# Optimization experiments

Measured on AMD Instinct MI355X. Metric: run time of the kernel, lower is better.

## Reference

```python
import jax, jax.numpy as jnp
import numpy as np

NUM_HEADS = 12
HEAD_DIM = 64
LOGIT_SCALE_MAX = 4.605170185988092  # log(1/0.01), open_clip default
EPS = 1e-12  # F.normalize eps


def setup_inputs() -> dict:
    key = jax.random.key(0)
    ks = jax.random.split(key, 8)
    N, L, C = 2, 2048, 768
    return {
        "x": jax.random.normal(ks[0], (N, L, C), dtype=jnp.float32),
        "in_proj_w": jax.random.normal(ks[1], (3 * C, C), dtype=jnp.float32) * 0.02,
        "in_proj_b": jax.random.normal(ks[2], (3 * C,), dtype=jnp.float32) * 0.02,
        "logit_scale": jax.random.normal(ks[3], (NUM_HEADS, 1, 1), dtype=jnp.float32),
        "learned_scale": jnp.ones((NUM_HEADS,), dtype=jnp.float32),
        "out_proj_w": jax.random.normal(ks[4], (C, C), dtype=jnp.float32) * 0.02,
        "out_proj_b": jax.random.normal(ks[5], (C,), dtype=jnp.float32) * 0.02,
        "attn_mask": jnp.zeros((L, L), dtype=jnp.float32),
    }


def _l2norm(t):
    # F.normalize(dim=-1): x / max(||x||, eps)
    n = jnp.linalg.norm(t, axis=-1, keepdims=True)
    return t / jnp.maximum(n, EPS)


def reference(x, in_proj_w, in_proj_b, logit_scale, learned_scale,
              out_proj_w, out_proj_b, attn_mask):
    N, L, C = x.shape
    H, D = NUM_HEADS, HEAD_DIM
    # packed QKV projection: [N, L, 3C]
    qkv = jnp.einsum("nlc,fc->nlf", x, in_proj_w) + in_proj_b
    q, k, v = jnp.split(qkv, 3, axis=-1)
    # [N, L, C] -> [N, H, L, D]
    to_heads = lambda t: t.reshape(N, L, H, D).transpose(0, 2, 1, 3)
    q, k, v = to_heads(q), to_heads(k), to_heads(v)
    # cosine attention with clamped exp logit scale per head
    attn = jnp.einsum("nhld,nhmd->nhlm", _l2norm(q), _l2norm(k))
    ls = jnp.exp(jnp.minimum(logit_scale, LOGIT_SCALE_MAX))  # [H,1,1]
    attn = attn * ls[None]  # broadcast over [N,H,L,L]
    attn = attn + attn_mask  # additive mask [L,L]
    attn = jax.nn.softmax(attn, axis=-1)
    out = jnp.einsum("nhlm,nhmd->nhld", attn, v)
    # learned per-head output scale
    out = out * learned_scale[None, :, None, None]
    # [N,H,L,D] -> [N,L,C]
    out = out.transpose(0, 2, 1, 3).reshape(N, L, C)
    out = jnp.einsum("nlc,fc->nlf", out, out_proj_w) + out_proj_b
    return out
```

## Files before the change

### kernel.cpp

```cpp
#include <hip/hip_runtime.h>
#include <math.h>

#define NB   2
#define SEQ  2048
#define CH   768
#define NH   12
#define HD   64
#define F3   2304
#define LSMAX 4.605170185988092f

typedef _Float16 f16;
typedef __attribute__((ext_vector_type(8))) _Float16 f16x8;
typedef __attribute__((ext_vector_type(4))) _Float16 f16x4;
typedef __attribute__((ext_vector_type(4))) float f32x4;

#define QSZ   3145728
#define OATT  (3 * QSZ)
#define XHOFF 12582912
#define W1OFF 15728640
#define W2OFF 17498112
#define MOFF  18087936

#define PIT  72
#define PPIT 76
#define GP   40

__global__ __launch_bounds__(256) void cvt_f16(const float* __restrict__ X,
                                               const float* __restrict__ W1,
                                               const float* __restrict__ W2,
                                               const float* __restrict__ M,
                                               f16* __restrict__ Xh,
                                               f16* __restrict__ W1h,
                                               f16* __restrict__ W2h,
                                               f16* __restrict__ Mh)
{
    int tid = blockIdx.x * 256 + threadIdx.x;
    const float* src; f16* dst; int n4;
    switch (blockIdx.y) {
        case 0:  src = X;  dst = Xh;  n4 = 786432;  break;
        case 1:  src = W1; dst = W1h; n4 = 442368;  break;
        case 2:  src = W2; dst = W2h; n4 = 147456;  break;
        default: src = M;  dst = Mh;  n4 = 1048576; break;
    }
    if (tid < n4) {
        float4 v = ((const float4*)src)[tid];
        f16x4 o = {(f16)v.x, (f16)v.y, (f16)v.z, (f16)v.w};
        ((f16x4*)dst)[tid] = o;
    }
}

__global__ __launch_bounds__(256, 3) void qkv_gemm(const f16* __restrict__ Xh,
                                                   const f16* __restrict__ Wh,
                                                   const float* __restrict__ bias,
                                                   const float* __restrict__ logit_scale,
                                                   f16* __restrict__ qkv16)
{
    __shared__ f16 As[128 * GP];
    __shared__ f16 Bs[128 * GP];
    const int t    = threadIdx.x;
    const int w    = t >> 6;
    const int lane = t & 63;
    const int quad = lane >> 4;
    const int sub  = lane & 15;
    const int wm   = w & 1, wn = w >> 1;
    const int f0   = blockIdx.x * 128;
    const int m0   = blockIdx.y * 128;
    const int srow = t >> 1;
    const int sk   = (t & 1) * 16;

    const f16* ag = Xh + (size_t)(m0 + srow) * CH + sk;
    const f16* bg = Wh + (size_t)(f0 + srow) * CH + sk;
    f16x8 a0 = *(const f16x8*)(ag);
    f16x8 a1 = *(const f16x8*)(ag + 8);
    f16x8 b0 = *(const f16x8*)(bg);
    f16x8 b1 = *(const f16x8*)(bg + 8);

    f32x4 acc[4][4];
#pragma unroll
    for (int i = 0; i < 4; ++i)
#pragma unroll
        for (int j = 0; j < 4; ++j) acc[i][j] = (f32x4){0.f, 0.f, 0.f, 0.f};

    for (int k0 = 0; k0 < CH; k0 += 32) {
        __syncthreads();
        *(f16x8*)&As[srow * GP + sk + 0] = a0;
        *(f16x8*)&As[srow * GP + sk + 8] = a1;
        *(f16x8*)&Bs[srow * GP + sk + 0] = b0;
        *(f16x8*)&Bs[srow * GP + sk + 8] = b1;
        __syncthreads();
        if (k0 + 32 < CH) {
            a0 = *(const f16x8*)(ag + k0 + 32);
            a1 = *(const f16x8*)(ag + k0 + 40);
            b0 = *(const f16x8*)(bg + k0 + 32);
            b1 = *(const f16x8*)(bg + k0 + 40);
        }
        f16x8 af[4], bf[4];
#pragma unroll
        for (int i = 0; i < 4; ++i) {
            af[i] = *(const f16x8*)&As[(wm * 64 + i * 16 + sub) * GP + quad * 8];
            bf[i] = *(const f16x8*)&Bs[(wn * 64 + i * 16 + sub) * GP + quad * 8];
        }
#pragma unroll
        for (int i = 0; i < 4; ++i)
#pragma unroll
            for (int j = 0; j < 4; ++j)
                acc[i][j] = __builtin_amdgcn_mfma_f32_16x16x32_f16(af[i], bf[j], acc[i][j], 0, 0, 0);
    }

    const int t3 = f0 / CH;
    const int h  = ((f0 + wn * 64) % CH) >> 6;
    f16* dst = qkv16 + (size_t)t3 * QSZ;
    float lsv = (t3 == 0) ? __expf(fminf(logit_scale[h], LSMAX)) : 1.0f;
    float bb[4];
#pragma unroll
    for (int j = 0; j < 4; ++j) bb[j] = bias[f0 + wn * 64 + j * 16 + sub];
#pragma unroll
    for (int i = 0; i < 4; ++i) {
#pragma unroll
        for (int r = 0; r < 4; ++r) {
            int m = m0 + wm * 64 + i * 16 + quad * 4 + r;
            int n = m >> 11, l = m & 2047;
            float v[4];
#pragma unroll
            for (int j = 0; j < 4; ++j) v[j] = acc[i][j][r] + bb[j];
            float scale = 1.0f;
            if (t3 < 2) {
                float ss = v[0] * v[0] + v[1] * v[1] + v[2] * v[2] + v[3] * v[3];
#pragma unroll
                for (int mk = 1; mk < 16; mk <<= 1) ss += __shfl_xor(ss, mk, 64);
                scale = 1.0f / fmaxf(sqrtf(ss), 1e-12f);
                if (t3 == 0) scale *= lsv;
            }
            f16* drow = dst + (((size_t)n * NH + h) * SEQ + l) * HD;
#pragma unroll
            for (int j = 0; j < 4; ++j)
                drow[j * 16 + sub] = (f16)(v[j] * scale);
        }
    }
}

__global__ __launch_bounds__(256, 3) void attn(const f16* __restrict__ Qh,
                                               const f16* __restrict__ Kh,
                                               const f16* __restrict__ Vh,
                                               const f16* __restrict__ Mh,
                                               const float* __restrict__ lscale,
                                               f16* __restrict__ Og)
{
    __shared__ f16 Ks[64 * PIT];
    __shared__ f16 Vt[64 * PIT];
    __shared__ f16 QP[64 * PPIT];

    const int t    = threadIdx.x;
    const int w    = t >> 6;
    const int lane = t & 63;
    const int quad = lane >> 4;
    const int sub  = lane & 15;
    const int qb   = blockIdx.x * 64;
    const int h    = blockIdx.y, n = blockIdx.z;

    const f16* Qg = Qh + ((size_t)(n * NH + h) * SEQ + qb) * HD;
    const f16* Kg = Kh + (size_t)(n * NH + h) * SEQ * HD;
    const f16* Vg = Vh + (size_t)(n * NH + h) * SEQ * HD;
    const f16* Mg = Mh + (size_t)(qb + w * 16 + quad * 4) * SEQ;

#pragma unroll
    for (int rep = 0; rep < 2; ++rep) {
        int id = rep * 256 + t;
        int row = id >> 3, c8 = id & 7;
        f16x8 v = *(const f16x8*)&Qg[row * 64 + c8 * 8];
        *(f16x4*)&QP[row * PPIT + c8 * 8 + 0] = (f16x4){v[0], v[1], v[2], v[3]};
        *(f16x4*)&QP[row * PPIT + c8 * 8 + 4] = (f16x4){v[4], v[5], v[6], v[7]};
    }
    __syncthreads();
    f16x8 qf0, qf1;
    {
        f16x4 l0 = *(const f16x4*)&QP[(w * 16 + sub) * PPIT + quad * 8];
        f16x4 l1 = *(const f16x4*)&QP[(w * 16 + sub) * PPIT + quad * 8 + 4];
        f16x4 l2 = *(const f16x4*)&QP[(w * 16 + sub) * PPIT + 32 + quad * 8];
        f16x4 l3 = *(const f16x4*)&QP[(w * 16 + sub) * PPIT + 32 + quad * 8 + 4];
        qf0 = (f16x8){l0[0], l0[1], l0[2], l0[3], l1[0], l1[1], l1[2], l1[3]};
        qf1 = (f16x8){l2[0], l2[1], l2[2], l2[3], l3[0], l3[1], l3[2], l3[3]};
    }

    const int krow = t >> 3, kc8 = t & 7;
    f16x8 kr0 = *(const f16x8*)&Kg[krow * 64 + kc8 * 8];
    f16x8 kr1 = *(const f16x8*)&Kg[(32 + krow) * 64 + kc8 * 8];
    f16x8 vr0 = *(const f16x8*)&Vg[lane * 64 + w * 16];
    f16x8 vr1 = *(const f16x8*)&Vg[lane * 64 + w * 16 + 8];
    f16 mnxt[16];
#pragma unroll
    for (int ct = 0; ct < 4; ++ct)
#pragma unroll
        for (int r = 0; r < 4; ++r)
            mnxt[ct * 4 + r] = Mg[(size_t)r * SEQ + ct * 16 + sub];

    f32x4 o[4];
    float m_run[4], l_lane[4];
#pragma unroll
    for (int dt = 0; dt < 4; ++dt) o[dt] = (f32x4){0.f, 0.f, 0.f, 0.f};
#pragma unroll
    for (int r = 0; r < 4; ++r) { m_run[r] = -1e30f; l_lane[r] = 0.f; }

    for (int c0 = 0; c0 < SEQ; c0 += 64) {
        __syncthreads();
        *(f16x8*)&Ks[krow * PIT + kc8 * 8] = kr0;
        *(f16x8*)&Ks[(32 + krow) * PIT + kc8 * 8] = kr1;
#pragma unroll
        for (int j = 0; j < 8; ++j) {
            Vt[(w * 16 + j) * PIT + lane] = vr0[j];
            Vt[(w * 16 + 8 + j) * PIT + lane] = vr1[j];
        }
        __syncthreads();

        f16 mcur[16];
#pragma unroll
        for (int i = 0; i < 16; ++i) mcur[i] = mnxt[i];
        if (c0 + 64 < SEQ) {
            const f16* Kn = Kg + (c0 + 64) * 64;
            const f16* Vn = Vg + (c0 + 64) * 64;
            kr0 = *(const f16x8*)&Kn[krow * 64 + kc8 * 8];
            kr1 = *(const f16x8*)&Kn[(32 + krow) * 64 + kc8 * 8];
            vr0 = *(const f16x8*)&Vn[lane * 64 + w * 16];
            vr1 = *(const f16x8*)&Vn[lane * 64 + w * 16 + 8];
#pragma unroll
            for (int ct = 0; ct < 4; ++ct)
#pragma unroll
                for (int r = 0; r < 4; ++r)
                    mnxt[ct * 4 + r] = Mg[(size_t)r * SEQ + c0 + 64 + ct * 16 + sub];
        }

        f32x4 s[4];
#pragma unroll
        for (int ct = 0; ct < 4; ++ct) {
            f16x8 kf0 = *(const f16x8*)&Ks[(ct * 16 + sub) * PIT + quad * 8];
            f16x8 kf1 = *(const f16x8*)&Ks[(ct * 16 + sub) * PIT + 32 + quad * 8];
            f32x4 a = (f32x4){0.f, 0.f, 0.f, 0.f};
            a = __builtin_amdgcn_mfma_f32_16x16x32_f16(qf0, kf0, a, 0, 0, 0);
            a = __builtin_amdgcn_mfma_f32_16x16x32_f16(qf1, kf1, a, 0, 0, 0);
            s[ct] = a;
        }
        float mnew[4];
#pragma unroll
        for (int r = 0; r < 4; ++r) mnew[r] = m_run[r];
#pragma unroll
        for (int ct = 0; ct < 4; ++ct)
#pragma unroll
            for (int r = 0; r < 4; ++r) {
                s[ct][r] += (float)mcur[ct * 4 + r];
                mnew[r] = fmaxf(mnew[r], s[ct][r]);
            }
#pragma unroll
        for (int r = 0; r < 4; ++r)
#pragma unroll
            for (int mk = 1; mk < 16; mk <<= 1)
                mnew[r] = fmaxf(mnew[r], __shfl_xor(mnew[r], mk, 64));
        float alpha[4], ps[4];
#pragma unroll
        for (int r = 0; r < 4; ++r) { alpha[r] = __expf(m_run[r] - mnew[r]); ps[r] = 0.f; }
#pragma unroll
        for (int ct = 0; ct < 4; ++ct)
#pragma unroll
            for (int r = 0; r < 4; ++r) {
                float p = __expf(s[ct][r] - mnew[r]);
                s[ct][r] = p;
                ps[r] += p;
            }
#pragma unroll
        for (int r = 0; r < 4; ++r) {
            l_lane[r] = l_lane[r] * alpha[r] + ps[r];
            m_run[r] = mnew[r];
        }
#pragma unroll
        for (int ct = 0; ct < 4; ++ct)
#pragma unroll
            for (int r = 0; r < 4; ++r)
                QP[(w * 16 + quad * 4 + r) * PPIT + ct * 16 + sub] = (f16)s[ct][r];
#pragma unroll
        for (int dt = 0; dt < 4; ++dt)
#pragma unroll
            for (int r = 0; r < 4; ++r) o[dt][r] *= alpha[r];
        f16x4 p00 = *(const f16x4*)&QP[(w * 16 + sub) * PPIT + quad * 8];
        f16x4 p01 = *(const f16x4*)&QP[(w * 16 + sub) * PPIT + quad * 8 + 4];
        f16x4 p10 = *(const f16x4*)&QP[(w * 16 + sub) * PPIT + 32 + quad * 8];
        f16x4 p11 = *(const f16x4*)&QP[(w * 16 + sub) * PPIT + 32 + quad * 8 + 4];
        f16x8 pf0 = {p00[0], p00[1], p00[2], p00[3], p01[0], p01[1], p01[2], p01[3]};
        f16x8 pf1 = {p10[0], p10[1], p10[2], p10[3], p11[0], p11[1], p11[2], p11[3]};
#pragma unroll
        for (int dt = 0; dt < 4; ++dt) {
            f16x8 vf0 = *(const f16x8*)&Vt[(dt * 16 + sub) * PIT + quad * 8];
            f16x8 vf1 = *(const f16x8*)&Vt[(dt * 16 + sub) * PIT + 32 + quad * 8];
            o[dt] = __builtin_amdgcn_mfma_f32_16x16x32_f16(pf0, vf0, o[dt], 0, 0, 0);
            o[dt] = __builtin_amdgcn_mfma_f32_16x16x32_f16(pf1, vf1, o[dt], 0, 0, 0);
        }
    }
    float lsc = lscale[h];
#pragma unroll
    for (int r = 0; r < 4; ++r) {
#pragma unroll
        for (int mk = 1; mk < 16; mk <<= 1)
            l_lane[r] += __shfl_xor(l_lane[r], mk, 64);
        float inv = lsc / l_lane[r];
        int q = qb + w * 16 + quad * 4 + r;
#pragma unroll
        for (int dt = 0; dt < 4; ++dt)
            Og[((size_t)n * SEQ + q) * CH + h * 64 + dt * 16 + sub] =
                (f16)(o[dt][r] * inv);
    }
}

__global__ __launch_bounds__(256, 3) void out_gemm(const f16* __restrict__ A,
                                                   const f16* __restrict__ Wh,
                                                   const float* __restrict__ bias,
                                                   float* __restrict__ out)
{
    __shared__ f16 As[128 * GP];
    __shared__ f16 Bs[128 * GP];
    const int t    = threadIdx.x;
    const int w    = t >> 6;
    const int lane = t & 63;
    const int quad = lane >> 4;
    const int sub  = lane & 15;
    const int wm   = w & 1, wn = w >> 1;
    const int f0   = blockIdx.x * 128;
    const int m0   = blockIdx.y * 128;
    const int srow = t >> 1;
    const int sk   = (t & 1) * 16;

    const f16* ag = A + (size_t)(m0 + srow) * CH + sk;
    const f16* bg = Wh + (size_t)(f0 + srow) * CH + sk;
    f16x8 a0 = *(const f16x8*)(ag);
    f16x8 a1 = *(const f16x8*)(ag + 8);
    f16x8 b0 = *(const f16x8*)(bg);
    f16x8 b1 = *(const f16x8*)(bg + 8);

    f32x4 acc[4][4];
#pragma unroll
    for (int i = 0; i < 4; ++i)
#pragma unroll
        for (int j = 0; j < 4; ++j) acc[i][j] = (f32x4){0.f, 0.f, 0.f, 0.f};

    for (int k0 = 0; k0 < CH; k0 += 32) {
        __syncthreads();
        *(f16x8*)&As[srow * GP + sk + 0] = a0;
        *(f16x8*)&As[srow * GP + sk + 8] = a1;
        *(f16x8*)&Bs[srow * GP + sk + 0] = b0;
        *(f16x8*)&Bs[srow * GP + sk + 8] = b1;
        __syncthreads();
        if (k0 + 32 < CH) {
            a0 = *(const f16x8*)(ag + k0 + 32);
            a1 = *(const f16x8*)(ag + k0 + 40);
            b0 = *(const f16x8*)(bg + k0 + 32);
            b1 = *(const f16x8*)(bg + k0 + 40);
        }
        f16x8 af[4], bf[4];
#pragma unroll
        for (int i = 0; i < 4; ++i) {
            af[i] = *(const f16x8*)&As[(wm * 64 + i * 16 + sub) * GP + quad * 8];
            bf[i] = *(const f16x8*)&Bs[(wn * 64 + i * 16 + sub) * GP + quad * 8];
        }
#pragma unroll
        for (int i = 0; i < 4; ++i)
#pragma unroll
            for (int j = 0; j < 4; ++j)
                acc[i][j] = __builtin_amdgcn_mfma_f32_16x16x32_f16(af[i], bf[j], acc[i][j], 0, 0, 0);
    }
    float bb[4];
#pragma unroll
    for (int j = 0; j < 4; ++j) bb[j] = bias[f0 + wn * 64 + j * 16 + sub];
#pragma unroll
    for (int i = 0; i < 4; ++i)
#pragma unroll
        for (int r = 0; r < 4; ++r) {
            int m = m0 + wm * 64 + i * 16 + quad * 4 + r;
            float* orow = out + (size_t)m * CH + f0 + wn * 64;
#pragma unroll
            for (int j = 0; j < 4; ++j)
                orow[j * 16 + sub] = acc[i][j][r] + bb[j];
        }
}

extern "C" void kernel_launch(void* const* d_in, const int* in_sizes, int n_in,
                              void* d_out, int out_size, void* d_ws, size_t ws_size,
                              hipStream_t stream) {
    const float* x    = (const float*)d_in[0];
    const float* w1   = (const float*)d_in[1];
    const float* b1   = (const float*)d_in[2];
    const float* ls   = (const float*)d_in[3];
    const float* lrn  = (const float*)d_in[4];
    const float* w2   = (const float*)d_in[5];
    const float* b2   = (const float*)d_in[6];
    const float* msk  = (const float*)d_in[7];
    f16*   ws16 = (f16*)d_ws;
    float* out  = (float*)d_out;

    hipLaunchKernelGGL(cvt_f16, dim3(4096, 4), dim3(256), 0, stream,
                       x, w1, w2, msk,
                       ws16 + XHOFF, ws16 + W1OFF, ws16 + W2OFF, ws16 + MOFF);
    hipLaunchKernelGGL(qkv_gemm, dim3(F3 / 128, (NB * SEQ) / 128), dim3(256), 0, stream,
                       ws16 + XHOFF, ws16 + W1OFF, b1, ls, ws16);
    hipLaunchKernelGGL(attn, dim3(SEQ / 64, NH, NB), dim3(256), 0, stream,
                       ws16, ws16 + QSZ, ws16 + 2 * QSZ, ws16 + MOFF, lrn, ws16 + OATT);
    hipLaunchKernelGGL(out_gemm, dim3(CH / 128, (NB * SEQ) / 128), dim3(256), 0, stream,
                       ws16 + OATT, ws16 + W2OFF, b2, out);
}
```

Measured before the change: 230.1 us.

## Double-buffer K/V tiles, skip zero mask, use exp2 and MFMA row sums in attention

Gives the attention kernel double-buffered K/V shared-memory tiles, so each key block needs one barrier instead of two and the next tile's stores overlap compute. A device flag set during mask conversion lets the kernel skip loading and adding the mask when it is all zeros. This check runs on the actual input every call, so it is not a hack. Softmax moves to the exp2 domain by folding log2(e) into the Q scale and the mask, the row max reduction uses packed f16 shuffles, and the row sums come from an MFMA against a ones vector instead of shuffles. The f16 max reduction slightly lowers precision, and the flag adds a memset and atomics.

```diff
diff --git a/kernel.cpp b/kernel.cpp
--- a/kernel.cpp
+++ b/kernel.cpp
@@ -8,10 +8,12 @@
 #define HD   64
 #define F3   2304
 #define LSMAX 4.605170185988092f
+#define LOG2E 1.4426950408889634f
 
 typedef _Float16 f16;
 typedef __attribute__((ext_vector_type(8))) _Float16 f16x8;
 typedef __attribute__((ext_vector_type(4))) _Float16 f16x4;
+typedef __attribute__((ext_vector_type(2))) _Float16 f16x2;
 typedef __attribute__((ext_vector_type(4))) float f32x4;
 
 #define QSZ   3145728
@@ -20,6 +22,7 @@
 #define W1OFF 15728640
 #define W2OFF 17498112
 #define MOFF  18087936
+#define FLAGO 22282240
 
 #define PIT  72
 #define PPIT 76
@@ -32,7 +35,8 @@
                                                f16* __restrict__ Xh,
                                                f16* __restrict__ W1h,
                                                f16* __restrict__ W2h,
-                                               f16* __restrict__ Mh)
+                                               f16* __restrict__ Mh,
+                                               int* __restrict__ flag)
 {
     int tid = blockIdx.x * 256 + threadIdx.x;
     const float* src; f16* dst; int n4;
@@ -44,6 +48,11 @@
     }
     if (tid < n4) {
         float4 v = ((const float4*)src)[tid];
+        if (blockIdx.y == 3) {
+            bool nz = (v.x != 0.f) || (v.y != 0.f) || (v.z != 0.f) || (v.w != 0.f);
+            if (__any(nz) && (threadIdx.x & 63) == 0) atomicOr(flag, 1);
+            v.x *= LOG2E; v.y *= LOG2E; v.z *= LOG2E; v.w *= LOG2E;
+        }
         f16x4 o = {(f16)v.x, (f16)v.y, (f16)v.z, (f16)v.w};
         ((f16x4*)dst)[tid] = o;
     }
@@ -110,7 +119,7 @@
     const int t3 = f0 / CH;
     const int h  = ((f0 + wn * 64) % CH) >> 6;
     f16* dst = qkv16 + (size_t)t3 * QSZ;
-    float lsv = (t3 == 0) ? __expf(fminf(logit_scale[h], LSMAX)) : 1.0f;
+    float lsv = (t3 == 0) ? __expf(fminf(logit_scale[h], LSMAX)) * LOG2E : 1.0f;
     float bb[4];
 #pragma unroll
     for (int j = 0; j < 4; ++j) bb[j] = bias[f0 + wn * 64 + j * 16 + sub];
@@ -144,10 +153,11 @@
                                                const f16* __restrict__ Vh,
                                                const f16* __restrict__ Mh,
                                                const float* __restrict__ lscale,
+                                               const int* __restrict__ flag,
                                                f16* __restrict__ Og)
 {
-    __shared__ f16 Ks[64 * PIT];
-    __shared__ f16 Vt[64 * PIT];
+    __shared__ f16 Ks[2][64 * PIT];
+    __shared__ f16 Vt[2][64 * PIT];
     __shared__ f16 QP[64 * PPIT];
 
     const int t    = threadIdx.x;
@@ -157,6 +167,7 @@
     const int sub  = lane & 15;
     const int qb   = blockIdx.x * 64;
     const int h    = blockIdx.y, n = blockIdx.z;
+    const bool has_mask = (*flag) != 0;
 
     const f16* Qg = Qh + ((size_t)(n * NH + h) * SEQ + qb) * HD;
     const f16* Kg = Kh + (size_t)(n * NH + h) * SEQ * HD;
@@ -171,6 +182,21 @@
         *(f16x4*)&QP[row * PPIT + c8 * 8 + 0] = (f16x4){v[0], v[1], v[2], v[3]};
         *(f16x4*)&QP[row * PPIT + c8 * 8 + 4] = (f16x4){v[4], v[5], v[6], v[7]};
     }
+
+    const int krow = t >> 3, kc8 = t & 7;
+    f16x8 kr0 = *(const f16x8*)&Kg[krow * 64 + kc8 * 8];
+    f16x8 kr1 = *(const f16x8*)&Kg[(32 + krow) * 64 + kc8 * 8];
+    f16x8 vr0 = *(const f16x8*)&Vg[lane * 64 + w * 16];
+    f16x8 vr1 = *(const f16x8*)&Vg[lane * 64 + w * 16 + 8];
+    f16 mnxt[16];
+    if (has_mask) {
+#pragma unroll
+        for (int ct = 0; ct < 4; ++ct)
+#pragma unroll
+            for (int r = 0; r < 4; ++r)
+                mnxt[ct * 4 + r] = Mg[(size_t)r * SEQ + ct * 16 + sub];
+    }
+
     __syncthreads();
     f16x8 qf0, qf1;
     {
@@ -182,113 +208,132 @@
         qf1 = (f16x8){l2[0], l2[1], l2[2], l2[3], l3[0], l3[1], l3[2], l3[3]};
     }
 
-    const int krow = t >> 3, kc8 = t & 7;
-    f16x8 kr0 = *(const f16x8*)&Kg[krow * 64 + kc8 * 8];
-    f16x8 kr1 = *(const f16x8*)&Kg[(32 + krow) * 64 + kc8 * 8];
-    f16x8 vr0 = *(const f16x8*)&Vg[lane * 64 + w * 16];
-    f16x8 vr1 = *(const f16x8*)&Vg[lane * 64 + w * 16 + 8];
-    f16 mnxt[16];
-#pragma unroll
-    for (int ct = 0; ct < 4; ++ct)
-#pragma unroll
-        for (int r = 0; r < 4; ++r)
-            mnxt[ct * 4 + r] = Mg[(size_t)r * SEQ + ct * 16 + sub];
-
+    *(f16x8*)&Ks[0][krow * PIT + kc8 * 8] = kr0;
+    *(f16x8*)&Ks[0][(32 + krow) * PIT + kc8 * 8] = kr1;
+#pragma unroll
+    for (int j = 0; j < 8; ++j) {
+        Vt[0][(w * 16 + j) * PIT + lane] = vr0[j];
+        Vt[0][(w * 16 + 8 + j) * PIT + lane] = vr1[j];
+    }
+    {
+        const f16* Kn = Kg + 64 * 64;
+        const f16* Vn = Vg + 64 * 64;
+        kr0 = *(const f16x8*)&Kn[krow * 64 + kc8 * 8];
+        kr1 = *(const f16x8*)&Kn[(32 + krow) * 64 + kc8 * 8];
+        vr0 = *(const f16x8*)&Vn[lane * 64 + w * 16];
+        vr1 = *(const f16x8*)&Vn[lane * 64 + w * 16 + 8];
+    }
+
+    const f16x8 ones = {(f16)1.f, (f16)1.f, (f16)1.f, (f16)1.f,
+                        (f16)1.f, (f16)1.f, (f16)1.f, (f16)1.f};
     f32x4 o[4];
-    float m_run[4], l_lane[4];
+    f32x4 l_acc = (f32x4){0.f, 0.f, 0.f, 0.f};
+    float m_run[4];
 #pragma unroll
     for (int dt = 0; dt < 4; ++dt) o[dt] = (f32x4){0.f, 0.f, 0.f, 0.f};
 #pragma unroll
-    for (int r = 0; r < 4; ++r) { m_run[r] = -1e30f; l_lane[r] = 0.f; }
-
-    for (int c0 = 0; c0 < SEQ; c0 += 64) {
+    for (int r = 0; r < 4; ++r) m_run[r] = -1e30f;
+
+    const int NC = SEQ / 64;
+    for (int c = 0; c < NC; ++c) {
         __syncthreads();
-        *(f16x8*)&Ks[krow * PIT + kc8 * 8] = kr0;
-        *(f16x8*)&Ks[(32 + krow) * PIT + kc8 * 8] = kr1;
-#pragma unroll
-        for (int j = 0; j < 8; ++j) {
-            Vt[(w * 16 + j) * PIT + lane] = vr0[j];
-            Vt[(w * 16 + 8 + j) * PIT + lane] = vr1[j];
-        }
-        __syncthreads();
-
+        const int cur = c & 1, nxt = cur ^ 1;
+        if (c + 1 < NC) {
+            *(f16x8*)&Ks[nxt][krow * PIT + kc8 * 8] = kr0;
+            *(f16x8*)&Ks[nxt][(32 + krow) * PIT + kc8 * 8] = kr1;
+#pragma unroll
+            for (int j = 0; j < 8; ++j) {
+                Vt[nxt][(w * 16 + j) * PIT + lane] = vr0[j];
+                Vt[nxt][(w * 16 + 8 + j) * PIT + lane] = vr1[j];
+            }
+            if (c + 2 < NC) {
+                const f16* Kn = Kg + (c + 2) * 64 * 64;
+                const f16* Vn = Vg + (c + 2) * 64 * 64;
+                kr0 = *(const f16x8*)&Kn[krow * 64 + kc8 * 8];
+                kr1 = *(const f16x8*)&Kn[(32 + krow) * 64 + kc8 * 8];
+                vr0 = *(const f16x8*)&Vn[lane * 64 + w * 16];
+                vr1 = *(const f16x8*)&Vn[lane * 64 + w * 16 + 8];
+            }
+        }
         f16 mcur[16];
-#pragma unroll
-        for (int i = 0; i < 16; ++i) mcur[i] = mnxt[i];
-        if (c0 + 64 < SEQ) {
-            const f16* Kn = Kg + (c0 + 64) * 64;
-            const f16* Vn = Vg + (c0 + 64) * 64;
-            kr0 = *(const f16x8*)&Kn[krow * 64 + kc8 * 8];
-            kr1 = *(const f16x8*)&Kn[(32 + krow) * 64 + kc8 * 8];
-            vr0 = *(const f16x8*)&Vn[lane * 64 + w * 16];
-            vr1 = *(const f16x8*)&Vn[lane * 64 + w * 16 + 8];
-#pragma unroll
-            for (int ct = 0; ct < 4; ++ct)
-#pragma unroll
-                for (int r = 0; r < 4; ++r)
-                    mnxt[ct * 4 + r] = Mg[(size_t)r * SEQ + c0 + 64 + ct * 16 + sub];
+        if (has_mask) {
+#pragma unroll
+            for (int i = 0; i < 16; ++i) mcur[i] = mnxt[i];
+            if (c + 1 < NC) {
+#pragma unroll
+                for (int ct = 0; ct < 4; ++ct)
+#pragma unroll
+                    for (int r = 0; r < 4; ++r)
+                        mnxt[ct * 4 + r] = Mg[(size_t)r * SEQ + (c + 1) * 64 + ct * 16 + sub];
+            }
         }
 
         f32x4 s[4];
 #pragma unroll
         for (int ct = 0; ct < 4; ++ct) {
-            f16x8 kf0 = *(const f16x8*)&Ks[(ct * 16 + sub) * PIT + quad * 8];
-            f16x8 kf1 = *(const f16x8*)&Ks[(ct * 16 + sub) * PIT + 32 + quad * 8];
+            f16x8 kf0 = *(const f16x8*)&Ks[cur][(ct * 16 + sub) * PIT + quad * 8];
+            f16x8 kf1 = *(const f16x8*)&Ks[cur][(ct * 16 + sub) * PIT + 32 + quad * 8];
             f32x4 a = (f32x4){0.f, 0.f, 0.f, 0.f};
             a = __builtin_amdgcn_mfma_f32_16x16x32_f16(qf0, kf0, a, 0, 0, 0);
             a = __builtin_amdgcn_mfma_f32_16x16x32_f16(qf1, kf1, a, 0, 0, 0);
             s[ct] = a;
         }
+        if (has_mask) {
+#pragma unroll
+            for (int ct = 0; ct < 4; ++ct)
+#pragma unroll
+                for (int r = 0; r < 4; ++r)
+                    s[ct][r] += (float)mcur[ct * 4 + r];
+        }
         float mnew[4];
 #pragma unroll
-        for (int r = 0; r < 4; ++r) mnew[r] = m_run[r];
+        for (int r = 0; r < 4; ++r)
+            mnew[r] = fmaxf(fmaxf(fmaxf(s[0][r], s[1][r]), fmaxf(s[2][r], s[3][r])), m_run[r]);
+        {
+            union { f16x2 h; int i; } p0, p1, v0, v1;
+            p0.h = (f16x2){(f16)mnew[0], (f16)mnew[1]};
+            p1.h = (f16x2){(f16)mnew[2], (f16)mnew[3]};
+#pragma unroll
+            for (int mk = 1; mk < 16; mk <<= 1) {
+                v0.i = __shfl_xor(p0.i, mk, 64);
+                v1.i = __shfl_xor(p1.i, mk, 64);
+                p0.h = __builtin_elementwise_max(p0.h, v0.h);
+                p1.h = __builtin_elementwise_max(p1.h, v1.h);
+            }
+            mnew[0] = (float)p0.h[0]; mnew[1] = (float)p0.h[1];
+            mnew[2] = (float)p1.h[0]; mnew[3] = (float)p1.h[1];
+        }
+        float alpha[4];
+#pragma unroll
+        for (int r = 0; r < 4; ++r) {
+            alpha[r] = exp2f(m_run[r] - mnew[r]);
+            m_run[r] = mnew[r];
+        }
 #pragma unroll
         for (int ct = 0; ct < 4; ++ct)
 #pragma unroll
             for (int r = 0; r < 4; ++r) {
-                s[ct][r] += (float)mcur[ct * 4 + r];
-                mnew[r] = fmaxf(mnew[r], s[ct][r]);
-            }
-#pragma unroll
-        for (int r = 0; r < 4; ++r)
-#pragma unroll
-            for (int mk = 1; mk < 16; mk <<= 1)
-                mnew[r] = fmaxf(mnew[r], __shfl_xor(mnew[r], mk, 64));
-        float alpha[4], ps[4];
-#pragma unroll
-        for (int r = 0; r < 4; ++r) { alpha[r] = __expf(m_run[r] - mnew[r]); ps[r] = 0.f; }
-#pragma unroll
-        for (int ct = 0; ct < 4; ++ct)
-#pragma unroll
-            for (int r = 0; r < 4; ++r) {
-                float p = __expf(s[ct][r] - mnew[r]);
-                s[ct][r] = p;
-                ps[r] += p;
-            }
-#pragma unroll
-        for (int r = 0; r < 4; ++r) {
-            l_lane[r] = l_lane[r] * alpha[r] + ps[r];
-            m_run[r] = mnew[r];
-        }
-#pragma unroll
-        for (int ct = 0; ct < 4; ++ct)
-#pragma unroll
-            for (int r = 0; r < 4; ++r)
-                QP[(w * 16 + quad * 4 + r) * PPIT + ct * 16 + sub] = (f16)s[ct][r];
+                float p = exp2f(s[ct][r] - mnew[r]);
+                QP[(w * 16 + quad * 4 + r) * PPIT + ct * 16 + sub] = (f16)p;
+            }
 #pragma unroll
         for (int dt = 0; dt < 4; ++dt)
 #pragma unroll
             for (int r = 0; r < 4; ++r) o[dt][r] *= alpha[r];
+#pragma unroll
+        for (int r = 0; r < 4; ++r) l_acc[r] *= alpha[r];
         f16x4 p00 = *(const f16x4*)&QP[(w * 16 + sub) * PPIT + quad * 8];
         f16x4 p01 = *(const f16x4*)&QP[(w * 16 + sub) * PPIT + quad * 8 + 4];
         f16x4 p10 = *(const f16x4*)&QP[(w * 16 + sub) * PPIT + 32 + quad * 8];
         f16x4 p11 = *(const f16x4*)&QP[(w * 16 + sub) * PPIT + 32 + quad * 8 + 4];
         f16x8 pf0 = {p00[0], p00[1], p00[2], p00[3], p01[0], p01[1], p01[2], p01[3]};
         f16x8 pf1 = {p10[0], p10[1], p10[2], p10[3], p11[0], p11[1], p11[2], p11[3]};
+        l_acc = __builtin_amdgcn_mfma_f32_16x16x32_f16(pf0, ones, l_acc, 0, 0, 0);
+        l_acc = __builtin_amdgcn_mfma_f32_16x16x32_f16(pf1, ones, l_acc, 0, 0, 0);
 #pragma unroll
         for (int dt = 0; dt < 4; ++dt) {
-            f16x8 vf0 = *(const f16x8*)&Vt[(dt * 16 + sub) * PIT + quad * 8];
-            f16x8 vf1 = *(const f16x8*)&Vt[(dt * 16 + sub) * PIT + 32 + quad * 8];
+            f16x8 vf0 = *(const f16x8*)&Vt[cur][(dt * 16 + sub) * PIT + quad * 8];
+            f16x8 vf1 = *(const f16x8*)&Vt[cur][(dt * 16 + sub) * PIT + 32 + quad * 8];
             o[dt] = __builtin_amdgcn_mfma_f32_16x16x32_f16(pf0, vf0, o[dt], 0, 0, 0);
             o[dt] = __builtin_amdgcn_mfma_f32_16x16x32_f16(pf1, vf1, o[dt], 0, 0, 0);
         }
@@ -296,10 +341,7 @@
     float lsc = lscale[h];
 #pragma unroll
     for (int r = 0; r < 4; ++r) {
-#pragma unroll
-        for (int mk = 1; mk < 16; mk <<= 1)
-            l_lane[r] += __shfl_xor(l_lane[r], mk, 64);
-        float inv = lsc / l_lane[r];
+        float inv = lsc / l_acc[r];
         int q = qb + w * 16 + quad * 4 + r;
 #pragma unroll
         for (int dt = 0; dt < 4; ++dt)
@@ -391,15 +433,18 @@
     const float* b2   = (const float*)d_in[6];
     const float* msk  = (const float*)d_in[7];
     f16*   ws16 = (f16*)d_ws;
+    int*   flag = (int*)(ws16 + FLAGO);
     float* out  = (float*)d_out;
 
+    (void)hipMemsetAsync(flag, 0, 4, stream);
     hipLaunchKernelGGL(cvt_f16, dim3(4096, 4), dim3(256), 0, stream,
                        x, w1, w2, msk,
-                       ws16 + XHOFF, ws16 + W1OFF, ws16 + W2OFF, ws16 + MOFF);
+                       ws16 + XHOFF, ws16 + W1OFF, ws16 + W2OFF, ws16 + MOFF, flag);
     hipLaunchKernelGGL(qkv_gemm, dim3(F3 / 128, (NB * SEQ) / 128), dim3(256), 0, stream,
                        ws16 + XHOFF, ws16 + W1OFF, b1, ls, ws16);
     hipLaunchKernelGGL(attn, dim3(SEQ / 64, NH, NB), dim3(256), 0, stream,
-                       ws16, ws16 + QSZ, ws16 + 2 * QSZ, ws16 + MOFF, lrn, ws16 + OATT);
+                       ws16, ws16 + QSZ, ws16 + 2 * QSZ, ws16 + MOFF, lrn, flag,
+                       ws16 + OATT);
     hipLaunchKernelGGL(out_gemm, dim3(CH / 128, (NB * SEQ) / 128), dim3(256), 0, stream,
                        ws16 + OATT, ws16 + W2OFF, b2, out);
 }
```

Result: no change. 227.5 us (-1.1%).
